# Optimization experiments

Measured on AMD Instinct MI355X. Metric: run time of the kernel, lower is better.

## Reference

```python
import jax, jax.numpy as jnp
import numpy as np

EPS = 1e-5
HEADS = 16
D_HEAD = 64
SCALE = D_HEAD ** -0.5


def layernorm(x, g, b):
    m = jnp.mean(x, axis=-1, keepdims=True)
    v = jnp.var(x, axis=-1, keepdims=True)
    return (x - m) * jax.lax.rsqrt(v + EPS) * g + b


def attention(x, ctx, Wq, Wk, Wv, Wo, bo):
    b, n, _ = x.shape
    m = ctx.shape[1]
    q = (x @ Wq).reshape(b, n, HEADS, D_HEAD)
    k = (ctx @ Wk).reshape(b, m, HEADS, D_HEAD)
    v = (ctx @ Wv).reshape(b, m, HEADS, D_HEAD)
    sim = jnp.einsum('bihd,bjhd->bhij', q, k) * SCALE  # [b,h,n,m]
    attn = jax.nn.softmax(sim, axis=-1)
    out = jnp.einsum('bhij,bjhd->bihd', attn, v).reshape(b, n, HEADS * D_HEAD)
    return out @ Wo + bo


def setup_inputs() -> dict:
    key = jax.random.key(0)
    ks = jax.random.split(key, 16)
    dim, ctx_dim, inner = 1024, 768, HEADS * D_HEAD
    ff_inner = 4 * dim
    s = lambda k, *sh: jax.random.normal(k, sh, jnp.float32) * 0.02
    return {
        'x': jax.random.normal(ks[0], (2, 2048, dim), jnp.float32),
        'context': jax.random.normal(ks[1], (2, 77, ctx_dim), jnp.float32),
        'ln1_g': jnp.ones((dim,), jnp.float32), 'ln1_b': jnp.zeros((dim,), jnp.float32),
        'a1_Wq': s(ks[2], dim, inner), 'a1_Wk': s(ks[3], dim, inner), 'a1_Wv': s(ks[4], dim, inner),
        'a1_Wo': s(ks[5], inner, dim), 'a1_bo': jnp.zeros((dim,), jnp.float32),
        'ln2_g': jnp.ones((dim,), jnp.float32), 'ln2_b': jnp.zeros((dim,), jnp.float32),
        'a2_Wq': s(ks[6], dim, inner), 'a2_Wk': s(ks[7], ctx_dim, inner), 'a2_Wv': s(ks[8], ctx_dim, inner),
        'a2_Wo': s(ks[9], inner, dim), 'a2_bo': jnp.zeros((dim,), jnp.float32),
        'ln3_g': jnp.ones((dim,), jnp.float32), 'ln3_b': jnp.zeros((dim,), jnp.float32),
        'ff_Wp': s(ks[10], dim, 2 * ff_inner), 'ff_bp': jnp.zeros((2 * ff_inner,), jnp.float32),
        'ff_Wo': s(ks[11], ff_inner, dim), 'ff_bo': jnp.zeros((dim,), jnp.float32),
    }


def reference(x, context, ln1_g, ln1_b, a1_Wq, a1_Wk, a1_Wv, a1_Wo, a1_bo,
              ln2_g, ln2_b, a2_Wq, a2_Wk, a2_Wv, a2_Wo, a2_bo,
              ln3_g, ln3_b, ff_Wp, ff_bp, ff_Wo, ff_bo):
    h = layernorm(x, ln1_g, ln1_b)
    x = attention(h, h, a1_Wq, a1_Wk, a1_Wv, a1_Wo, a1_bo) + x
    h = layernorm(x, ln2_g, ln2_b)
    x = attention(h, context, a2_Wq, a2_Wk, a2_Wv, a2_Wo, a2_bo) + x
    h = layernorm(x, ln3_g, ln3_b)
    p = h @ ff_Wp + ff_bp
    u, gate = jnp.split(p, 2, axis=-1)
    ff = (u * jax.nn.gelu(gate, approximate=False)) @ ff_Wo + ff_bo
    return ff + x
```

## Files before the change

### kernel.cpp

```cpp
#include <hip/hip_runtime.h>
#include <hip/hip_bf16.h>

typedef __hip_bfloat16 bf16;
typedef short s16x8 __attribute__((ext_vector_type(8)));
typedef float f32x4 __attribute__((ext_vector_type(4)));

#define NSEQ 2048
#define DIM  1024
#define CTXD 768
#define INNER 1024
#define NH 16
#define DH 64
#define NB 2
#define TOK (NB*NSEQ)
#define MCTX 77
#define CTOK (NB*MCTX)
#define VSTR_X 128

__device__ __forceinline__ void gload_lds16(const void* g, void* lds) {
  __builtin_amdgcn_global_load_lds(
      (const __attribute__((address_space(1))) unsigned int*)g,
      (__attribute__((address_space(3))) unsigned int*)lds, 16, 0, 0);
}

__device__ __forceinline__ void wtile(float (*tile)[33], const float* __restrict__ W,
                                      bf16* __restrict__ WT, int K, int N, int t, int REMAP) {
  const int nkx = K >> 5;
  const int kx = t % nkx, ny = t / nkx;
  const int r = threadIdx.x >> 5, c = threadIdx.x & 31;
  const int k0 = kx * 32, n0 = ny * 32;
#pragma unroll
  for (int i = 0; i < 4; ++i)
    tile[r + i*8][c] = W[(size_t)(k0 + r + i*8) * N + n0 + c];
  __syncthreads();
#pragma unroll
  for (int i = 0; i < 4; ++i) {
    int n = n0 + r + i*8;
    if (REMAP == 2) {
      const int f = (n < 4096) ? n : n - 4096;
      n = ((f >> 5) << 6) + ((n < 4096) ? 0 : 32) + (f & 31);
    }
    WT[(size_t)n * K + k0 + c] = __float2bfloat16(tile[c][r + i*8]);
  }
}

#define PB1  1024
#define PB2  2048
#define PB3  3072
#define PB4  4096
#define PB5  5120
#define PB6  5888
#define PB7  6656
#define PB8  7680
#define PB9  15872
#define PB10 19968
#define PB11 20430
#define PB12 20462
#define PTOT 20590

__global__ __launch_bounds__(256)
void prep_kernel(const float* __restrict__ Wq1, const float* __restrict__ Wk1,
                 const float* __restrict__ Wv1, const float* __restrict__ Wo1,
                 const float* __restrict__ Wq2, const float* __restrict__ Wk2,
                 const float* __restrict__ Wv2, const float* __restrict__ Wo2,
                 const float* __restrict__ Wp,  const float* __restrict__ Wf,
                 const float* __restrict__ bp,  const float* __restrict__ ctx,
                 bf16* wqkvT, bf16* wo1T, bf16* wq2T, bf16* wkv2T, bf16* wo2T,
                 bf16* wpT, bf16* wfT, float* bpi, bf16* ctxb, float4* vz) {
  __shared__ float tile[32][33];
  const int bid = blockIdx.x;
  if (bid < PB1)        wtile(tile, Wq1, wqkvT,                         1024, 1024, bid,        0);
  else if (bid < PB2)   wtile(tile, Wk1, wqkvT + (size_t)1024 * 1024,   1024, 1024, bid - PB1,  0);
  else if (bid < PB3)   wtile(tile, Wv1, wqkvT + (size_t)2048 * 1024,   1024, 1024, bid - PB2,  0);
  else if (bid < PB4)   wtile(tile, Wo1, wo1T,                          1024, 1024, bid - PB3,  0);
  else if (bid < PB5)   wtile(tile, Wq2, wq2T,                          1024, 1024, bid - PB4,  0);
  else if (bid < PB6)   wtile(tile, Wk2, wkv2T,                          768, 1024, bid - PB5,  0);
  else if (bid < PB7)   wtile(tile, Wv2, wkv2T + (size_t)1024 * 768,     768, 1024, bid - PB6,  0);
  else if (bid < PB8)   wtile(tile, Wo2, wo2T,                          1024, 1024, bid - PB7,  0);
  else if (bid < PB9)   wtile(tile, Wp,  wpT,                           1024, 8192, bid - PB8,  2);
  else if (bid < PB10)  wtile(tile, Wf,  wfT,                           4096, 1024, bid - PB9,  0);
  else if (bid < PB11) {
    const int i = (bid - PB10) * 256 + threadIdx.x;
    ctxb[i] = __float2bfloat16(ctx[i]);
  } else if (bid < PB12) {
    const int i = (bid - PB11) * 256 + threadIdx.x;
    const int f = (i < 4096) ? i : i - 4096;
    const int n = ((f >> 5) << 6) + ((i < 4096) ? 0 : 32) + (f & 31);
    bpi[n] = bp[i];
  } else {
    const int i = (bid - PB12) * 256 + threadIdx.x;
    vz[i] = make_float4(0.f, 0.f, 0.f, 0.f);
  }
}

__global__ __launch_bounds__(256)
void ln_kernel(const float* __restrict__ x, const float* __restrict__ gw,
               const float* __restrict__ bw, bf16* __restrict__ out) {
  const int row = blockIdx.x;
  const int t = threadIdx.x;
  const float4 xv = ((const float4*)(x + (size_t)row * DIM))[t];
  float s = xv.x + xv.y + xv.z + xv.w;
  float q = xv.x*xv.x + xv.y*xv.y + xv.z*xv.z + xv.w*xv.w;
#pragma unroll
  for (int m = 1; m < 64; m <<= 1) { s += __shfl_xor(s, m); q += __shfl_xor(q, m); }
  __shared__ float red[8];
  const int lane = t & 63, w = t >> 6;
  if (lane == 0) { red[w] = s; red[4 + w] = q; }
  __syncthreads();
  s = red[0] + red[1] + red[2] + red[3];
  q = red[4] + red[5] + red[6] + red[7];
  const float mean = s * (1.f / DIM);
  const float var = q * (1.f / DIM) - mean * mean;
  const float rs = rsqrtf(var + 1e-5f);
  const float4 gv = ((const float4*)gw)[t];
  const float4 bv = ((const float4*)bw)[t];
  union { bf16 h[4]; uint2 u; } o;
  o.h[0] = __float2bfloat16((xv.x - mean) * rs * gv.x + bv.x);
  o.h[1] = __float2bfloat16((xv.y - mean) * rs * gv.y + bv.y);
  o.h[2] = __float2bfloat16((xv.z - mean) * rs * gv.z + bv.z);
  o.h[3] = __float2bfloat16((xv.w - mean) * rs * gv.w + bv.w);
  ((uint2*)(out + (size_t)row * DIM))[t] = o.u;
}

template<int EPI, int BN>
__global__ __launch_bounds__(256)
void gemm_bt(const bf16* __restrict__ A, const bf16* __restrict__ Bt,
             void* __restrict__ o0, void* __restrict__ o1, void* __restrict__ o2,
             const float* __restrict__ bias, const float* __restrict__ resid,
             int M, int Nn, int K, float scale) {
  constexpr int NT = BN / 32;
  __shared__ bf16 Als[128 * 64];
  __shared__ bf16 Bls[BN * 64];
  const int tid = threadIdx.x;
  const int lane = tid & 63;
  const int w = tid >> 6;
  const int g = lane >> 4, r16 = lane & 15;
  const int tm = blockIdx.x * 128, tn = blockIdx.y * BN;
  const int wm = (w >> 1) * 64, wn = (w & 1) * (BN / 2);

  f32x4 acc[4][NT];
#pragma unroll
  for (int i = 0; i < 4; ++i)
#pragma unroll
    for (int j = 0; j < NT; ++j) acc[i][j] = (f32x4){0.f, 0.f, 0.f, 0.f};

  for (int kt = 0; kt < K; kt += 64) {
    __syncthreads();
#pragma unroll
    for (int i = 0; i < 4; ++i) {
      const int slot = (w * 4 + i) * 64 + lane;
      const int row = slot >> 3;
      const int sch = (slot & 7) ^ (row & 7);
      int ar = tm + row; ar = ar < M ? ar : M - 1;
      gload_lds16(A + (size_t)ar * K + kt + sch * 8, (char*)Als + (w * 4 + i) * 1024);
    }
#pragma unroll
    for (int i = 0; i < NT; ++i) {
      const int slot = (w * NT + i) * 64 + lane;
      const int row = slot >> 3;
      const int sch = (slot & 7) ^ (row & 7);
      gload_lds16(Bt + (size_t)(tn + row) * K + kt + sch * 8, (char*)Bls + (w * NT + i) * 1024);
    }
    __syncthreads();
#pragma unroll
    for (int kk = 0; kk < 2; ++kk) {
      s16x8 af[4], bfr[NT];
#pragma unroll
      for (int mt = 0; mt < 4; ++mt) {
        const int row = wm + mt * 16 + r16;
        const int ch = (kk * 4 + g) ^ (row & 7);
        af[mt] = *(const s16x8*)((const char*)Als + row * 128 + ch * 16);
      }
#pragma unroll
      for (int nt = 0; nt < NT; ++nt) {
        const int row = wn + nt * 16 + r16;
        const int ch = (kk * 4 + g) ^ (row & 7);
        bfr[nt] = *(const s16x8*)((const char*)Bls + row * 128 + ch * 16);
      }
#pragma unroll
      for (int mt = 0; mt < 4; ++mt)
#pragma unroll
        for (int nt = 0; nt < NT; ++nt)
          acc[mt][nt] = __builtin_amdgcn_mfma_f32_16x16x32_bf16(af[mt], bfr[nt], acc[mt][nt], 0, 0, 0);
    }
  }

  if constexpr (EPI == 4) {
    const int base = tn + wn;
#pragma unroll
    for (int nt = 0; nt < 2; ++nt) {
      const int cu = base + nt * 16 + r16;
      const float bu = bias[cu];
      const float bg = bias[cu + 32];
      const int f = (base >> 1) + nt * 16 + r16;
#pragma unroll
      for (int mt = 0; mt < 4; ++mt) {
        const int row0 = tm + wm + mt * 16 + 4 * g;
#pragma unroll
        for (int j = 0; j < 4; ++j) {
          const float u  = acc[mt][nt][j] + bu;
          const float gg = acc[mt][nt + 2][j] + bg;
          const float ge = 0.5f * gg * (1.f + erff(gg * 0.70710678118654752f));
          ((bf16*)o0)[(size_t)(row0 + j) * (Nn >> 1) + f] = __float2bfloat16(u * ge);
        }
      }
    }
  } else {
#pragma unroll
    for (int mt = 0; mt < 4; ++mt) {
      const int row0 = tm + wm + mt * 16 + 4 * g;
#pragma unroll
      for (int nt = 0; nt < NT; ++nt) {
        const int col = tn + wn + nt * 16 + r16;
#pragma unroll
        for (int j = 0; j < 4; ++j) {
          const int row = row0 + j;
          if (row >= M) continue;
          const float v = acc[mt][nt][j];
          if (EPI == 0) {
            ((bf16*)o0)[(size_t)row * Nn + col] = __float2bfloat16(v * scale);
          } else if (EPI == 2) {
            ((float*)o0)[(size_t)row * Nn + col] = v + bias[col] + resid[(size_t)row * Nn + col];
          } else if (EPI == 5) {
            const int seg = tn >> 10;
            const int lcol = col - (seg << 10);
            if (seg == 0) {
              ((bf16*)o0)[(size_t)row * INNER + lcol] = __float2bfloat16(v * 0.125f);
            } else if (seg == 1) {
              ((bf16*)o1)[(size_t)row * INNER + lcol] = __float2bfloat16(v);
            } else {
              const int b = row >> 11, i = row & (NSEQ - 1);
              ((bf16*)o2)[((size_t)(b * INNER + lcol)) * NSEQ + i] = __float2bfloat16(v);
            }
          } else if (EPI == 6) {
            const int seg = tn >> 10;
            const int lcol = col - (seg << 10);
            if (seg == 0) {
              ((bf16*)o0)[(size_t)row * INNER + lcol] = __float2bfloat16(v);
            } else {
              const int b = row / MCTX, i = row - b * MCTX;
              ((bf16*)o2)[((size_t)(b * INNER + lcol)) * VSTR_X + i] = __float2bfloat16(v);
            }
          }
        }
      }
    }
  }
}

__global__ __launch_bounds__(256)
void attn_kernel(const bf16* __restrict__ q, const bf16* __restrict__ k,
                 const bf16* __restrict__ vT, bf16* __restrict__ out,
                 int m_kv, int vstr) {
  __shared__ bf16 Kls[64 * 64];
  __shared__ bf16 Vls[80 * 64];
  __shared__ bf16 Pls[4][32 * 64];

  const int tid = threadIdx.x, lane = tid & 63, w = tid >> 6;
  const int g = lane >> 4, r16 = lane & 15;
  const int qt = blockIdx.x, h = blockIdx.y, b = blockIdx.z;

  s16x8 qf[2][2];
#pragma unroll
  for (int mt = 0; mt < 2; ++mt) {
    const int qrow = qt * 128 + w * 32 + mt * 16 + r16;
    const bf16* qb_ = q + ((size_t)(b * NSEQ + qrow)) * INNER + h * DH;
    qf[mt][0] = *(const s16x8*)(qb_ + 8 * g);
    qf[mt][1] = *(const s16x8*)(qb_ + 32 + 8 * g);
  }

  {
    const unsigned int ones2 = 0x3F803F80u;
    uint2 val;
    val.x = (tid < 16) ? ones2 : 0u;
    val.y = val.x;
    *(uint2*)((char*)Vls + 64 * 128 + tid * 8) = val;
  }

  f32x4 acc[2][5];
#pragma unroll
  for (int mt = 0; mt < 2; ++mt)
#pragma unroll
    for (int nt = 0; nt < 5; ++nt) acc[mt][nt] = (f32x4){0.f, 0.f, 0.f, 0.f};

  const int ntiles = (m_kv + 63) >> 6;
  int4 kreg[2], vreg[2];

  auto prefetch = [&](int kt) {
#pragma unroll
    for (int i = 0; i < 2; ++i) {
      const int slot = i * 256 + tid;
      const int row = slot >> 3;
      const int sch = (slot & 7) ^ (row & 7);
      const int key = kt * 64 + row;
      kreg[i] = (key < m_kv)
          ? *(const int4*)(k + ((size_t)(b * m_kv + key)) * INNER + h * DH + sch * 8)
          : (int4){0, 0, 0, 0};
      vreg[i] = *(const int4*)(vT + ((size_t)(b * INNER + h * DH + row)) * vstr + kt * 64 + sch * 8);
    }
  };

  prefetch(0);
  bf16* pw = &Pls[w][0];

  for (int kt = 0; kt < ntiles; ++kt) {
    const bool full = (kt * 64 + 64) <= m_kv;
    __syncthreads();
#pragma unroll
    for (int i = 0; i < 2; ++i) {
      const int slot = i * 256 + tid;
      *(int4*)((char*)Kls + slot * 16) = kreg[i];
      *(int4*)((char*)Vls + slot * 16) = vreg[i];
    }
    __syncthreads();
    if (kt + 1 < ntiles) prefetch(kt + 1);

    f32x4 s4[2][4];
#pragma unroll
    for (int mt = 0; mt < 2; ++mt)
#pragma unroll
      for (int nt = 0; nt < 4; ++nt) s4[mt][nt] = (f32x4){0.f, 0.f, 0.f, 0.f};
#pragma unroll
    for (int kk = 0; kk < 2; ++kk) {
      s16x8 kf[4];
#pragma unroll
      for (int nt = 0; nt < 4; ++nt) {
        const int row = nt * 16 + r16;
        const int ch = (kk * 4 + g) ^ (row & 7);
        kf[nt] = *(const s16x8*)((const char*)Kls + row * 128 + ch * 16);
      }
#pragma unroll
      for (int mt = 0; mt < 2; ++mt)
#pragma unroll
        for (int nt = 0; nt < 4; ++nt)
          s4[mt][nt] = __builtin_amdgcn_mfma_f32_16x16x32_bf16(qf[mt][kk], kf[nt], s4[mt][nt], 0, 0, 0);
    }
    if (!full) {
#pragma unroll
      for (int nt = 0; nt < 4; ++nt) {
        const int key = kt * 64 + nt * 16 + r16;
        if (key >= m_kv) {
#pragma unroll
          for (int mt = 0; mt < 2; ++mt) {
            s4[mt][nt][0] = -1e30f; s4[mt][nt][1] = -1e30f;
            s4[mt][nt][2] = -1e30f; s4[mt][nt][3] = -1e30f;
          }
        }
      }
    }

#pragma unroll
    for (int mt = 0; mt < 2; ++mt) {
#pragma unroll
      for (int j = 0; j < 4; ++j) {
        const int prow = mt * 16 + 4 * g + j;
        const int rowbase = prow * 128;
        const int sw = (prow & 7) << 4;
#pragma unroll
        for (int nt = 0; nt < 4; ++nt) {
          const float p = __expf(s4[mt][nt][j]);
          const int byte = rowbase + ((nt * 32 + r16 * 2) ^ sw);
          *(bf16*)((char*)pw + byte) = __float2bfloat16(p);
        }
      }
    }

#pragma unroll
    for (int kk = 0; kk < 2; ++kk) {
      s16x8 vf[5];
#pragma unroll
      for (int nt = 0; nt < 5; ++nt) {
        const int row = nt * 16 + r16;
        const int ch = (kk * 4 + g) ^ (row & 7);
        vf[nt] = *(const s16x8*)((const char*)Vls + row * 128 + ch * 16);
      }
#pragma unroll
      for (int mt = 0; mt < 2; ++mt) {
        const int prow = mt * 16 + r16;
        const int pch = (kk * 4 + g) ^ (prow & 7);
        const s16x8 pa = *(const s16x8*)((const char*)pw + prow * 128 + pch * 16);
#pragma unroll
        for (int nt = 0; nt < 5; ++nt)
          acc[mt][nt] = __builtin_amdgcn_mfma_f32_16x16x32_bf16(pa, vf[nt], acc[mt][nt], 0, 0, 0);
      }
    }
  }

#pragma unroll
  for (int mt = 0; mt < 2; ++mt) {
#pragma unroll
    for (int j = 0; j < 4; ++j) {
      const float rs = 1.f / __shfl(acc[mt][4][j], lane & 48);
      const int row = qt * 128 + w * 32 + mt * 16 + 4 * g + j;
#pragma unroll
      for (int nt = 0; nt < 4; ++nt) {
        const int col = h * DH + nt * 16 + r16;
        out[((size_t)(b * NSEQ + row)) * INNER + col] = __float2bfloat16(acc[mt][nt][j] * rs);
      }
    }
  }
}

extern "C" void kernel_launch(void* const* d_in, const int* in_sizes, int n_in,
                              void* d_out, int out_size, void* d_ws, size_t ws_size,
                              hipStream_t stream) {
  const float* x    = (const float*)d_in[0];
  const float* ctx  = (const float*)d_in[1];
  const float* ln1g = (const float*)d_in[2];
  const float* ln1b = (const float*)d_in[3];
  const float* Wq1  = (const float*)d_in[4];
  const float* Wk1  = (const float*)d_in[5];
  const float* Wv1  = (const float*)d_in[6];
  const float* Wo1  = (const float*)d_in[7];
  const float* bo1  = (const float*)d_in[8];
  const float* ln2g = (const float*)d_in[9];
  const float* ln2b = (const float*)d_in[10];
  const float* Wq2  = (const float*)d_in[11];
  const float* Wk2  = (const float*)d_in[12];
  const float* Wv2  = (const float*)d_in[13];
  const float* Wo2  = (const float*)d_in[14];
  const float* bo2  = (const float*)d_in[15];
  const float* ln3g = (const float*)d_in[16];
  const float* ln3b = (const float*)d_in[17];
  const float* Wp   = (const float*)d_in[18];
  const float* bp   = (const float*)d_in[19];
  const float* Wf   = (const float*)d_in[20];
  const float* bfo  = (const float*)d_in[21];

  char* ws = (char*)d_ws;
  size_t off = 0;
  auto alloc = [&](size_t bytes) { char* p = ws + off; off += (bytes + 255) & ~(size_t)255; return p; };
  bf16* wqkvT = (bf16*)alloc((size_t)3072 * 1024 * 2);
  bf16* wo1T  = (bf16*)alloc((size_t)1024 * 1024 * 2);
  bf16* wq2T  = (bf16*)alloc((size_t)1024 * 1024 * 2);
  bf16* wkv2T = (bf16*)alloc((size_t)2048 * 768 * 2);
  bf16* wo2T  = (bf16*)alloc((size_t)1024 * 1024 * 2);
  bf16* wpT   = (bf16*)alloc((size_t)8192 * 1024 * 2);
  bf16* wfT   = (bf16*)alloc((size_t)1024 * 4096 * 2);
  float* bpi  = (float*)alloc((size_t)8192 * 4);
  bf16* ctxb  = (bf16*)alloc((size_t)CTOK * CTXD * 2);
  bf16* hb    = (bf16*)alloc((size_t)TOK * DIM * 2);
  bf16* qb    = (bf16*)alloc((size_t)TOK * INNER * 2);
  bf16* kb    = (bf16*)alloc((size_t)TOK * INNER * 2);
  bf16* vTb   = (bf16*)alloc((size_t)NB * INNER * NSEQ * 2);
  bf16* vTb2  = (bf16*)alloc((size_t)NB * INNER * VSTR_X * 2);
  bf16* ao    = (bf16*)alloc((size_t)TOK * INNER * 2);
  float* xbuf = (float*)alloc((size_t)TOK * DIM * 4);
  bf16* ffin  = (bf16*)alloc((size_t)TOK * 4096 * 2);

  const dim3 blk(256);
  prep_kernel<<<dim3(PTOT), blk, 0, stream>>>(Wq1, Wk1, Wv1, Wo1, Wq2, Wk2, Wv2, Wo2,
                                              Wp, Wf, bp, ctx,
                                              wqkvT, wo1T, wq2T, wkv2T, wo2T,
                                              wpT, wfT, bpi, ctxb, (float4*)vTb2);

  ln_kernel<<<dim3(TOK), blk, 0, stream>>>(x, ln1g, ln1b, hb);
  gemm_bt<5, 128><<<dim3(32, 24), blk, 0, stream>>>(hb, wqkvT, qb, kb, vTb, nullptr, nullptr, TOK, 3072, 1024, 1.f);
  attn_kernel<<<dim3(16, 16, 2), blk, 0, stream>>>(qb, kb, vTb, ao, NSEQ, NSEQ);
  gemm_bt<2, 64><<<dim3(32, 16), blk, 0, stream>>>(ao, wo1T, xbuf, nullptr, nullptr, bo1, x, TOK, 1024, 1024, 1.f);

  ln_kernel<<<dim3(TOK), blk, 0, stream>>>(xbuf, ln2g, ln2b, hb);
  gemm_bt<0, 64><<<dim3(32, 16), blk, 0, stream>>>(hb, wq2T, qb, nullptr, nullptr, nullptr, nullptr, TOK, 1024, 1024, 0.125f);
  gemm_bt<6, 64><<<dim3(2, 32), blk, 0, stream>>>(ctxb, wkv2T, kb, nullptr, vTb2, nullptr, nullptr, CTOK, 2048, 768, 1.f);
  attn_kernel<<<dim3(16, 16, 2), blk, 0, stream>>>(qb, kb, vTb2, ao, MCTX, VSTR_X);
  gemm_bt<2, 64><<<dim3(32, 16), blk, 0, stream>>>(ao, wo2T, xbuf, nullptr, nullptr, bo2, xbuf, TOK, 1024, 1024, 1.f);

  ln_kernel<<<dim3(TOK), blk, 0, stream>>>(xbuf, ln3g, ln3b, hb);
  gemm_bt<4, 128><<<dim3(32, 64), blk, 0, stream>>>(hb, wpT, ffin, nullptr, nullptr, bpi, nullptr, TOK, 8192, 1024, 1.f);
  gemm_bt<2, 64><<<dim3(32, 16), blk, 0, stream>>>(ffin, wfT, (float*)d_out, nullptr, nullptr, bfo, xbuf, TOK, 1024, 4096, 1.f);

  (void)in_sizes; (void)n_in; (void)out_size; (void)ws_size;
}
```

Measured before the change: 538.8 us.

## Double-buffer GEMM LDS tiles and use register ones-fragment for attention row sums

The GEMM now keeps two LDS buffers for A and B tiles. It issues the global-to-LDS loads for the next K tile before computing on the current one, waiting with a vmcnt counter instead of a full sync before every load, so memory latency can overlap with MFMA work. In the attention kernel, the extra 16 rows of ones that were stored in LDS to compute softmax row sums are replaced by a constant register fragment fed straight into the MFMA. This trims LDS use and a few reads. The GEMM change doubles its shared memory, which may lower occupancy, and adds a second barrier per iteration.

```diff
diff --git a/kernel.cpp b/kernel.cpp
--- a/kernel.cpp
+++ b/kernel.cpp
@@ -129,8 +129,9 @@
              const float* __restrict__ bias, const float* __restrict__ resid,
              int M, int Nn, int K, float scale) {
   constexpr int NT = BN / 32;
-  __shared__ bf16 Als[128 * 64];
-  __shared__ bf16 Bls[BN * 64];
+  constexpr int LPT = 4 + NT;
+  __shared__ bf16 Als[2][128 * 64];
+  __shared__ bf16 Bls[2][BN * 64];
   const int tid = threadIdx.x;
   const int lane = tid & 63;
   const int w = tid >> 6;
@@ -144,24 +145,38 @@
 #pragma unroll
     for (int j = 0; j < NT; ++j) acc[i][j] = (f32x4){0.f, 0.f, 0.f, 0.f};
 
-  for (int kt = 0; kt < K; kt += 64) {
-    __syncthreads();
+  auto stage = [&](int kt, int buf) {
 #pragma unroll
     for (int i = 0; i < 4; ++i) {
       const int slot = (w * 4 + i) * 64 + lane;
       const int row = slot >> 3;
       const int sch = (slot & 7) ^ (row & 7);
       int ar = tm + row; ar = ar < M ? ar : M - 1;
-      gload_lds16(A + (size_t)ar * K + kt + sch * 8, (char*)Als + (w * 4 + i) * 1024);
+      gload_lds16(A + (size_t)ar * K + kt + sch * 8, (char*)Als[buf] + (w * 4 + i) * 1024);
     }
 #pragma unroll
     for (int i = 0; i < NT; ++i) {
       const int slot = (w * NT + i) * 64 + lane;
       const int row = slot >> 3;
       const int sch = (slot & 7) ^ (row & 7);
-      gload_lds16(Bt + (size_t)(tn + row) * K + kt + sch * 8, (char*)Bls + (w * NT + i) * 1024);
-    }
-    __syncthreads();
+      gload_lds16(Bt + (size_t)(tn + row) * K + kt + sch * 8, (char*)Bls[buf] + (w * NT + i) * 1024);
+    }
+  };
+
+  const int ntk = K >> 6;
+  stage(0, 0);
+  for (int tk = 0; tk < ntk; ++tk) {
+    const int cur = tk & 1;
+    if (tk + 1 < ntk) {
+      stage((tk + 1) << 6, cur ^ 1);
+      asm volatile("s_waitcnt vmcnt(%0)" :: "i"(LPT) : "memory");
+    } else {
+      asm volatile("s_waitcnt vmcnt(0)" ::: "memory");
+    }
+    __builtin_amdgcn_s_barrier();
+    __builtin_amdgcn_sched_barrier(0);
+    const char* als = (const char*)Als[cur];
+    const char* bls = (const char*)Bls[cur];
 #pragma unroll
     for (int kk = 0; kk < 2; ++kk) {
       s16x8 af[4], bfr[NT];
@@ -169,13 +184,13 @@
       for (int mt = 0; mt < 4; ++mt) {
         const int row = wm + mt * 16 + r16;
         const int ch = (kk * 4 + g) ^ (row & 7);
-        af[mt] = *(const s16x8*)((const char*)Als + row * 128 + ch * 16);
+        af[mt] = *(const s16x8*)(als + row * 128 + ch * 16);
       }
 #pragma unroll
       for (int nt = 0; nt < NT; ++nt) {
         const int row = wn + nt * 16 + r16;
         const int ch = (kk * 4 + g) ^ (row & 7);
-        bfr[nt] = *(const s16x8*)((const char*)Bls + row * 128 + ch * 16);
+        bfr[nt] = *(const s16x8*)(bls + row * 128 + ch * 16);
       }
 #pragma unroll
       for (int mt = 0; mt < 4; ++mt)
@@ -183,6 +198,8 @@
         for (int nt = 0; nt < NT; ++nt)
           acc[mt][nt] = __builtin_amdgcn_mfma_f32_16x16x32_bf16(af[mt], bfr[nt], acc[mt][nt], 0, 0, 0);
     }
+    __builtin_amdgcn_s_barrier();
+    __builtin_amdgcn_sched_barrier(0);
   }
 
   if constexpr (EPI == 4) {
@@ -253,7 +270,7 @@
                  const bf16* __restrict__ vT, bf16* __restrict__ out,
                  int m_kv, int vstr) {
   __shared__ bf16 Kls[64 * 64];
-  __shared__ bf16 Vls[80 * 64];
+  __shared__ bf16 Vls[64 * 64];
   __shared__ bf16 Pls[4][32 * 64];
 
   const int tid = threadIdx.x, lane = tid & 63, w = tid >> 6;
@@ -269,13 +286,8 @@
     qf[mt][1] = *(const s16x8*)(qb_ + 32 + 8 * g);
   }
 
-  {
-    const unsigned int ones2 = 0x3F803F80u;
-    uint2 val;
-    val.x = (tid < 16) ? ones2 : 0u;
-    val.y = val.x;
-    *(uint2*)((char*)Vls + 64 * 128 + tid * 8) = val;
-  }
+  const short ov = (r16 == 0) ? (short)0x3F80 : (short)0;
+  const s16x8 onesf = {ov, ov, ov, ov, ov, ov, ov, ov};
 
   f32x4 acc[2][5];
 #pragma unroll
@@ -367,9 +379,9 @@
 
 #pragma unroll
     for (int kk = 0; kk < 2; ++kk) {
-      s16x8 vf[5];
-#pragma unroll
-      for (int nt = 0; nt < 5; ++nt) {
+      s16x8 vf[4];
+#pragma unroll
+      for (int nt = 0; nt < 4; ++nt) {
         const int row = nt * 16 + r16;
         const int ch = (kk * 4 + g) ^ (row & 7);
         vf[nt] = *(const s16x8*)((const char*)Vls + row * 128 + ch * 16);
@@ -380,8 +392,9 @@
         const int pch = (kk * 4 + g) ^ (prow & 7);
         const s16x8 pa = *(const s16x8*)((const char*)pw + prow * 128 + pch * 16);
 #pragma unroll
-        for (int nt = 0; nt < 5; ++nt)
+        for (int nt = 0; nt < 4; ++nt)
           acc[mt][nt] = __builtin_amdgcn_mfma_f32_16x16x32_bf16(pa, vf[nt], acc[mt][nt], 0, 0, 0);
+        acc[mt][4] = __builtin_amdgcn_mfma_f32_16x16x32_bf16(pa, onesf, acc[mt][4], 0, 0, 0);
       }
     }
   }
```

Result: slower. 560.5 us (+4.0%).
